# Optimization experiments

Measured on AMD Instinct MI355X. Metric: run time of the kernel, lower is better.

## Reference

```python
import jax, jax.numpy as jnp
import numpy as np

B, S, D_MODEL = 4, 2048, 128
NUM_HEADS, HEAD_DIM = 4, 32
EPS = 1e-6


def setup_inputs() -> dict:
    key = jax.random.key(0)
    ks = jax.random.split(key, 5)
    scale = 1.0 / np.sqrt(D_MODEL)
    return {
        "x": jax.random.normal(ks[0], (B, S, D_MODEL), dtype=jnp.float32),
        "Wq": jax.random.normal(ks[1], (D_MODEL, NUM_HEADS * HEAD_DIM), dtype=jnp.float32) * scale,
        "bq": jnp.zeros((NUM_HEADS * HEAD_DIM,), dtype=jnp.float32),
        "Wk": jax.random.normal(ks[2], (D_MODEL, NUM_HEADS * HEAD_DIM), dtype=jnp.float32) * scale,
        "bk": jnp.zeros((NUM_HEADS * HEAD_DIM,), dtype=jnp.float32),
        "Wv": jax.random.normal(ks[3], (D_MODEL, NUM_HEADS * HEAD_DIM), dtype=jnp.float32) * scale,
        "bv": jnp.zeros((NUM_HEADS * HEAD_DIM,), dtype=jnp.float32),
        "gamma": jnp.ones((D_MODEL,), dtype=jnp.float32),
        "beta": jnp.zeros((D_MODEL,), dtype=jnp.float32),
        "Wo": jax.random.normal(ks[4], (NUM_HEADS * HEAD_DIM, D_MODEL), dtype=jnp.float32) * scale,
        "bo": jnp.zeros((D_MODEL,), dtype=jnp.float32),
    }


def _split_heads(t):
    # [B, S, H*D] -> [B, H, S, D]
    b, s, _ = t.shape
    return t.reshape(b, s, NUM_HEADS, HEAD_DIM).transpose(0, 2, 1, 3)


def reference(x, Wq, bq, Wk, bk, Wv, bv, gamma, beta, Wo, bo):
    # Pre-LayerNorm (Keras LayerNormalization, eps=1e-6)
    mu = jnp.mean(x, axis=-1, keepdims=True)
    var = jnp.mean(jnp.square(x - mu), axis=-1, keepdims=True)
    xn = (x - mu) * jax.lax.rsqrt(var + EPS) * gamma + beta

    q = _split_heads(xn @ Wq + bq)  # [B,H,S,Dh]
    k = _split_heads(xn @ Wk + bk)
    v = _split_heads(xn @ Wv + bv)

    scores = jnp.einsum("bhqd,bhkd->bhqk", q, k) / jnp.sqrt(jnp.float32(HEAD_DIM))
    attn = jax.nn.softmax(scores, axis=-1)  # [B,H,S,S]
    ctx = jnp.einsum("bhqk,bhkd->bhqd", attn, v)  # [B,H,S,Dh]

    # merge heads -> [B,S,H*Dh]
    ctx = ctx.transpose(0, 2, 1, 3).reshape(x.shape[0], x.shape[1], NUM_HEADS * HEAD_DIM)
    out = ctx @ Wo + bo
    return out + x  # residual
```

## Files before the change

### kernel.cpp

```cpp
#include <hip/hip_runtime.h>

#define D_MODEL 128
#define SEQ 2048
#define NH 4
#define DH 32
#define NBATCH 4
#define BHN 16

typedef __attribute__((ext_vector_type(8))) short bf16x8;
typedef __attribute__((ext_vector_type(4))) float f32x4;
typedef __attribute__((ext_vector_type(4))) unsigned short u16x4;
typedef __attribute__((ext_vector_type(8))) unsigned short u16x8;

#define QSCALE (0.17677669529663687f * 1.4426950408889634f)

static __device__ __forceinline__ unsigned short f2bf_rne(float f) {
    union { float f; unsigned int u; } v; v.f = f;
    unsigned int r = v.u + 0x7FFFu + ((v.u >> 16) & 1u);
    return (unsigned short)(r >> 16);
}


__global__ __launch_bounds__(512) void k1_ln_qkv(
    const float* __restrict__ x,
    const float* __restrict__ Wq, const float* __restrict__ Wk,
    const float* __restrict__ Wv,
    const float* __restrict__ bq, const float* __restrict__ bk,
    const float* __restrict__ bv,
    const float* __restrict__ gamma, const float* __restrict__ beta,
    unsigned short* __restrict__ qf_ws, unsigned short* __restrict__ kf_ws,
    unsigned short* __restrict__ vf_ws)
{
    __shared__ __align__(16) unsigned short wsh[96 * 512];
    __shared__ __align__(16) unsigned short xsh[32][136];
    __shared__ __align__(16) unsigned short stqk[32][272];
    __shared__ __align__(16) unsigned short stv[128][40];
    const int t = threadIdx.x, w = t >> 6, lane = t & 63;
    const int col = lane & 15, quad = lane >> 4;
    const int row0 = blockIdx.x * 32;
    const float g0 = gamma[lane], g1 = gamma[lane + 64];
    const float be0 = beta[lane], be1 = beta[lane + 64];
    #pragma unroll
    for (int i = 0; i < 4; ++i) {
        int r = w * 4 + i;
        const float* xr = x + (size_t)(row0 + r) * 128;
        float x0 = xr[lane], x1 = xr[lane + 64];
        float s = x0 + x1, s2 = x0 * x0 + x1 * x1;
        #pragma unroll
        for (int off = 32; off > 0; off >>= 1) {
            s += __shfl_xor(s, off);
            s2 += __shfl_xor(s2, off);
        }
        float mu  = s * (1.0f / 128.0f);
        float var = s2 * (1.0f / 128.0f) - mu * mu;
        float rs  = rsqrtf(var + 1e-6f);
        xsh[r][lane]      = f2bf_rne((x0 - mu) * rs * g0 + be0);
        xsh[r][lane + 64] = f2bf_rne((x1 - mu) * rs * g1 + be1);
    }

    #pragma unroll
    for (int i = 0; i < 12; ++i) {
        int u = w * 12 + i;
        int nt = u >> 2, kk = u & 3;
        const float* W = (nt < 8) ? Wq : (nt < 16) ? Wk : Wv;
        int n = (nt & 7) * 16 + col;
        u16x8 v;
        #pragma unroll
        for (int j = 0; j < 8; ++j)
            v[j] = f2bf_rne(W[(kk * 32 + quad * 8 + j) * 128 + n]);
        *(u16x8*)&wsh[(size_t)u * 512 + lane * 8] = v;
    }
    __syncthreads();

    const int mt = w & 1, mrow = mt * 16;
    const int nt0 = (w >> 1) * 6;
    bf16x8 a[4];
    #pragma unroll
    for (int kk = 0; kk < 4; ++kk)
        a[kk] = *(const bf16x8*)&xsh[mrow + col][kk * 32 + quad * 8];

    for (int nt = nt0; nt < nt0 + 6; ++nt) {
        int n = nt * 16 + col;
        f32x4 c = {0.f, 0.f, 0.f, 0.f};
        #pragma unroll
        for (int kk = 0; kk < 4; ++kk) {
            bf16x8 bfr = *(const bf16x8*)&wsh[(size_t)(nt * 4 + kk) * 512 + lane * 8];
            c = __builtin_amdgcn_mfma_f32_16x16x32_bf16(a[kk], bfr, c, 0, 0, 0);
        }
        int m = nt >> 3;
        int nn = n & 127;
        if (m < 2) {
            float bias = (m == 0) ? bq[nn] : bk[nn];
            float scale = (m == 0) ? QSCALE : 1.0f;
            #pragma unroll
            for (int r = 0; r < 4; ++r)
                stqk[mrow + quad * 4 + r][n] = f2bf_rne((c[r] + bias) * scale);
        } else {
            float bias = bv[nn];
            u16x4 pv;
            #pragma unroll
            for (int r = 0; r < 4; ++r) pv[r] = f2bf_rne(c[r] + bias);
            *(u16x4*)&stv[nn][mrow + quad * 4] = pv;
        }
    }
    __syncthreads();

    const int b   = row0 >> 11;
    const int kbi = (row0 & (SEQ - 1)) >> 5;
    const int h   = w >> 1, par = w & 1;
    const int bh  = b * NH + h;
    {
        u16x8 qv = *(const u16x8*)&stqk[par * 16 + col][h * 32 + quad * 8];
        int qi = ((row0 & (SEQ - 1)) >> 4) + par;
        *(u16x8*)(qf_ws + (size_t)(bh * 128 + qi) * 512 + lane * 8) = qv;
    }
    {
        u16x8 kv = *(const u16x8*)&stqk[2 * col + par][128 + h * 32 + quad * 8];
        *(u16x8*)(kf_ws + ((size_t)(bh * 64 + kbi) * 2 + par) * 512 + lane * 8) = kv;
    }
    {
        u16x8 vv = *(const u16x8*)&stv[h * 32 + par * 16 + col][quad * 8];
        *(u16x8*)(vf_ws + ((size_t)(bh * 64 + kbi) * 2 + par) * 512 + lane * 8) = vv;
    }
}

__global__ __launch_bounds__(1024) void k23_attn_out(
    const unsigned short* __restrict__ qf_ws,
    const unsigned short* __restrict__ kf_ws,
    const unsigned short* __restrict__ vf_ws,
    const float* __restrict__ Wo,
    const float* __restrict__ bo, const float* __restrict__ x,
    float* __restrict__ out)
{
    __shared__ __align__(16) unsigned short wo_sh[32 * 512];
    __shared__ __align__(16) float comb[16][32][33];
    __shared__ float lsh[16][32];
    __shared__ __align__(16) unsigned short ctx_sh[32][136];

    const int w = threadIdx.x >> 6, lane = threadIdx.x & 63;
    const int col = lane & 15, quad = lane >> 4;
    const int h = w >> 2, kh = w & 3;
    const int b = blockIdx.y;
    const int bh = b * NH + h;
    const int q0 = blockIdx.x * 32;
    const int qi = blockIdx.x * 2;

    #pragma unroll
    for (int i = 0; i < 2; ++i) {
        int u = w * 2 + i;
        int nt = u >> 2, kk = u & 3;
        int n = nt * 16 + col;
        u16x8 vv;
        #pragma unroll
        for (int j = 0; j < 8; ++j)
            vv[j] = f2bf_rne(Wo[(kk * 32 + quad * 8 + j) * 128 + n]);
        *(u16x8*)&wo_sh[(size_t)u * 512 + lane * 8] = vv;
    }

    const unsigned short* qb = qf_ws + (size_t)(bh * 128 + qi) * 512;
    const unsigned short* kb0 = kf_ws + (size_t)bh * 65536 + (size_t)(kh * 16) * 1024;
    const unsigned short* vb0 = vf_ws + (size_t)bh * 65536 + (size_t)(kh * 16) * 1024;

    bf16x8 qf0 = *(const bf16x8*)(qb + lane * 8);
    bf16x8 qf1 = *(const bf16x8*)(qb + 512 + lane * 8);

    f32x4 c00 = {0.f,0.f,0.f,0.f}, c01 = {0.f,0.f,0.f,0.f};
    f32x4 c10 = {0.f,0.f,0.f,0.f}, c11 = {0.f,0.f,0.f,0.f};
    float l0 = 0.f, l1 = 0.f;

    const unsigned short* pk = kb0;
    const unsigned short* pv = vb0;
    bf16x8 kf0 = *(const bf16x8*)(pk + lane * 8);
    bf16x8 kf1 = *(const bf16x8*)(pk + 512 + lane * 8);
    bf16x8 vf0 = *(const bf16x8*)(pv + lane * 8);
    bf16x8 vf1 = *(const bf16x8*)(pv + 512 + lane * 8);

    for (int it = 0; it < 16; ++it) {
        const unsigned short* nk = (it == 15) ? kb0 : pk + 1024;
        const unsigned short* nv = (it == 15) ? vb0 : pv + 1024;
        bf16x8 nkf0 = *(const bf16x8*)(nk + lane * 8);
        bf16x8 nkf1 = *(const bf16x8*)(nk + 512 + lane * 8);
        bf16x8 nvf0 = *(const bf16x8*)(nv + lane * 8);
        bf16x8 nvf1 = *(const bf16x8*)(nv + 512 + lane * 8);

        f32x4 z = {0.f,0.f,0.f,0.f};
        __builtin_amdgcn_s_setprio(1);
        f32x4 s00 = __builtin_amdgcn_mfma_f32_16x16x32_bf16(kf0, qf0, z, 0, 0, 0);
        f32x4 s01 = __builtin_amdgcn_mfma_f32_16x16x32_bf16(kf1, qf0, z, 0, 0, 0);
        f32x4 s10 = __builtin_amdgcn_mfma_f32_16x16x32_bf16(kf0, qf1, z, 0, 0, 0);
        f32x4 s11 = __builtin_amdgcn_mfma_f32_16x16x32_bf16(kf1, qf1, z, 0, 0, 0);
        __builtin_amdgcn_s_setprio(0);

        union { bf16x8 v; unsigned int u[4]; } pf0, pf1;
        #pragma unroll
        for (int r = 0; r < 4; ++r) {
            float pe = __builtin_amdgcn_exp2f(s00[r]);
            float po = __builtin_amdgcn_exp2f(s01[r]);
            l0 += pe + po;
            pf0.u[r] = (__float_as_uint(pe) >> 16) | (__float_as_uint(po) & 0xFFFF0000u);
            float qe = __builtin_amdgcn_exp2f(s10[r]);
            float qo = __builtin_amdgcn_exp2f(s11[r]);
            l1 += qe + qo;
            pf1.u[r] = (__float_as_uint(qe) >> 16) | (__float_as_uint(qo) & 0xFFFF0000u);
        }
        __builtin_amdgcn_s_setprio(1);
        c00 = __builtin_amdgcn_mfma_f32_16x16x32_bf16(pf0.v, vf0, c00, 0, 0, 0);
        c01 = __builtin_amdgcn_mfma_f32_16x16x32_bf16(pf0.v, vf1, c01, 0, 0, 0);
        c10 = __builtin_amdgcn_mfma_f32_16x16x32_bf16(pf1.v, vf0, c10, 0, 0, 0);
        c11 = __builtin_amdgcn_mfma_f32_16x16x32_bf16(pf1.v, vf1, c11, 0, 0, 0);
        __builtin_amdgcn_s_setprio(0);
        kf0 = nkf0; kf1 = nkf1; vf0 = nvf0; vf1 = nvf1;
        pk = nk; pv = nv;
    }

    l0 += __shfl_xor(l0, 16); l0 += __shfl_xor(l0, 32);
    l1 += __shfl_xor(l1, 16); l1 += __shfl_xor(l1, 32);

    #pragma unroll
    for (int r = 0; r < 4; ++r) {
        int rr = quad * 4 + r;
        comb[w][rr][col]           = c00[r];
        comb[w][rr][16 + col]      = c01[r];
        comb[w][16 + rr][col]      = c10[r];
        comb[w][16 + rr][16 + col] = c11[r];
    }
    if (quad == 0) {
        lsh[w][col]      = l0;
        lsh[w][16 + col] = l1;
    }
    __syncthreads();

    {
        int row = threadIdx.x >> 5;
        int dg  = (threadIdx.x & 31) * 4;
        int hh  = dg >> 5;
        int wb  = hh * 4;
        float linv = 1.0f / (lsh[wb][row] + lsh[wb + 1][row]
                           + lsh[wb + 2][row] + lsh[wb + 3][row]);
        int dl = dg & 31;
        u16x4 ov;
        #pragma unroll
        for (int j = 0; j < 4; ++j)
            ov[j] = f2bf_rne((comb[wb][row][dl + j] + comb[wb + 1][row][dl + j]
                            + comb[wb + 2][row][dl + j] + comb[wb + 3][row][dl + j])
                             * linv);
        *(u16x4*)&ctx_sh[row][dg] = ov;
    }
    __syncthreads();

    {
        int nt = w & 7, mt = w >> 3;
        bf16x8 a[4];
        #pragma unroll
        for (int kk = 0; kk < 4; ++kk)
            a[kk] = *(const bf16x8*)&ctx_sh[mt * 16 + col][kk * 32 + quad * 8];
        int n = nt * 16 + col;
        f32x4 c = {0.f, 0.f, 0.f, 0.f};
        #pragma unroll
        for (int kk = 0; kk < 4; ++kk) {
            bf16x8 bfr = *(const bf16x8*)&wo_sh[(size_t)(nt * 4 + kk) * 512 + lane * 8];
            c = __builtin_amdgcn_mfma_f32_16x16x32_bf16(a[kk], bfr, c, 0, 0, 0);
        }
        float bias = bo[n];
        #pragma unroll
        for (int r = 0; r < 4; ++r) {
            size_t row_g = (size_t)b * SEQ + q0 + mt * 16 + quad * 4 + r;
            out[row_g * 128 + n] = c[r] + bias + x[row_g * 128 + n];
        }
    }
}

extern "C" void kernel_launch(void* const* d_in, const int* in_sizes, int n_in,
                              void* d_out, int out_size, void* d_ws, size_t ws_size,
                              hipStream_t stream) {
    const float* x     = (const float*)d_in[0];
    const float* Wq    = (const float*)d_in[1];
    const float* bq    = (const float*)d_in[2];
    const float* Wk    = (const float*)d_in[3];
    const float* bk    = (const float*)d_in[4];
    const float* Wv    = (const float*)d_in[5];
    const float* bv    = (const float*)d_in[6];
    const float* gamma = (const float*)d_in[7];
    const float* beta  = (const float*)d_in[8];
    const float* Wo    = (const float*)d_in[9];
    const float* bo    = (const float*)d_in[10];
    float* out = (float*)d_out;

    const size_t QKV_ELEMS = (size_t)BHN * SEQ * DH;
    unsigned short* qf_ws = (unsigned short*)d_ws;
    unsigned short* kf_ws = qf_ws + QKV_ELEMS;
    unsigned short* vf_ws = kf_ws + QKV_ELEMS;

    k1_ln_qkv<<<256, 512, 0, stream>>>(x, Wq, Wk, Wv, bq, bk, bv, gamma, beta,
                                       qf_ws, kf_ws, vf_ws);
    k23_attn_out<<<dim3(64, 4), 1024, 0, stream>>>(qf_ws, kf_ws, vf_ws, Wo,
                                                   bo, x, out);
}
```

Baseline: 100.2 us.

## Swizzle blocks across XCDs per batch and use packed bf16 conversion

Both kernels move to a 1D grid. Block IDs are remapped so that all blocks working on one batch land on the same pair of XCDs, which is meant to keep that batch's K/V and x rows resident in the shared L2. The LayerNorm stage now loads x, gamma and beta as float2 and writes packed bf16 pairs. The softmax probability packing swaps manual truncation for the hardware round-to-nearest pack2 conversion, which slightly changes rounding and may lower ALU cost in the inner loop.

```diff
diff --git a/kernel.cpp b/kernel.cpp
--- a/kernel.cpp
+++ b/kernel.cpp
@@ -1,4 +1,5 @@
 #include <hip/hip_runtime.h>
+#include <hip/hip_bf16.h>
 
 #define D_MODEL 128
 #define SEQ 2048
@@ -18,6 +19,13 @@
     union { float f; unsigned int u; } v; v.f = f;
     unsigned int r = v.u + 0x7FFFu + ((v.u >> 16) & 1u);
     return (unsigned short)(r >> 16);
+}
+
+static __device__ __forceinline__ unsigned int pack2_bf16(float lo, float hi) {
+    float2 t; t.x = lo; t.y = hi;
+    union { __hip_bfloat162 b; unsigned int u; } cv;
+    cv.b = __float22bfloat162_rn(t);
+    return cv.u;
 }
 
 
@@ -37,14 +45,21 @@
     __shared__ __align__(16) unsigned short stv[128][40];
     const int t = threadIdx.x, w = t >> 6, lane = t & 63;
     const int col = lane & 15, quad = lane >> 4;
-    const int row0 = blockIdx.x * 32;
-    const float g0 = gamma[lane], g1 = gamma[lane + 64];
-    const float be0 = beta[lane], be1 = beta[lane + 64];
+
+    const int bid = blockIdx.x;
+    const int xcd = bid & 7, slot = bid >> 3;
+    const int bsw = xcd >> 1;
+    const int rblk = (xcd & 1) * 32 + slot;
+    const int row0 = bsw * SEQ + rblk * 32;
+
+    const float2 gg = ((const float2*)gamma)[lane];
+    const float2 bb = ((const float2*)beta)[lane];
     #pragma unroll
     for (int i = 0; i < 4; ++i) {
         int r = w * 4 + i;
         const float* xr = x + (size_t)(row0 + r) * 128;
-        float x0 = xr[lane], x1 = xr[lane + 64];
+        float2 xp = ((const float2*)xr)[lane];
+        float x0 = xp.x, x1 = xp.y;
         float s = x0 + x1, s2 = x0 * x0 + x1 * x1;
         #pragma unroll
         for (int off = 32; off > 0; off >>= 1) {
@@ -54,8 +69,9 @@
         float mu  = s * (1.0f / 128.0f);
         float var = s2 * (1.0f / 128.0f) - mu * mu;
         float rs  = rsqrtf(var + 1e-6f);
-        xsh[r][lane]      = f2bf_rne((x0 - mu) * rs * g0 + be0);
-        xsh[r][lane + 64] = f2bf_rne((x1 - mu) * rs * g1 + be1);
+        *(unsigned int*)&xsh[r][lane * 2] =
+            pack2_bf16((x0 - mu) * rs * gg.x + bb.x,
+                       (x1 - mu) * rs * gg.y + bb.y);
     }
 
     #pragma unroll
@@ -140,10 +156,14 @@
     const int w = threadIdx.x >> 6, lane = threadIdx.x & 63;
     const int col = lane & 15, quad = lane >> 4;
     const int h = w >> 2, kh = w & 3;
-    const int b = blockIdx.y;
+
+    const int bid = blockIdx.x;
+    const int xcd = bid & 7, slot = bid >> 3;
+    const int b = xcd >> 1;
+    const int qib = (xcd & 1) * 32 + slot;
     const int bh = b * NH + h;
-    const int q0 = blockIdx.x * 32;
-    const int qi = blockIdx.x * 2;
+    const int q0 = qib * 32;
+    const int qi = qib * 2;
 
     #pragma unroll
     for (int i = 0; i < 2; ++i) {
@@ -197,11 +217,11 @@
             float pe = __builtin_amdgcn_exp2f(s00[r]);
             float po = __builtin_amdgcn_exp2f(s01[r]);
             l0 += pe + po;
-            pf0.u[r] = (__float_as_uint(pe) >> 16) | (__float_as_uint(po) & 0xFFFF0000u);
+            pf0.u[r] = pack2_bf16(pe, po);
             float qe = __builtin_amdgcn_exp2f(s10[r]);
             float qo = __builtin_amdgcn_exp2f(s11[r]);
             l1 += qe + qo;
-            pf1.u[r] = (__float_as_uint(qe) >> 16) | (__float_as_uint(qo) & 0xFFFF0000u);
+            pf1.u[r] = pack2_bf16(qe, qo);
         }
         __builtin_amdgcn_s_setprio(1);
         c00 = __builtin_amdgcn_mfma_f32_16x16x32_bf16(pf0.v, vf0, c00, 0, 0, 0);
@@ -293,6 +313,6 @@
 
     k1_ln_qkv<<<256, 512, 0, stream>>>(x, Wq, Wk, Wv, bq, bk, bv, gamma, beta,
                                        qf_ws, kf_ws, vf_ws);
-    k23_attn_out<<<dim3(64, 4), 1024, 0, stream>>>(qf_ws, kf_ws, vf_ws, Wo,
-                                                   bo, x, out);
-}
+    k23_attn_out<<<256, 1024, 0, stream>>>(qf_ws, kf_ws, vf_ws, Wo,
+                                           bo, x, out);
+}
```

New measurement: 103.2 us. +2.9%, slower.

## Fuse LN-QKV and attention kernels into one cooperative kernel with grid sync

Applied to the files above, without the earlier changes.

Merges the LayerNorm+QKV projection kernel and the attention+output-projection kernel into a single cooperative launch of 256 blocks of 1024 threads, separated by a grid-wide barrier. Shared memory is aliased between the two phases, and the Wo staging is done before the barrier to overlap with the QKV writes. This removes one kernel launch and the gap between kernels. In exchange it adds a grid sync and requires all 256 blocks to be co-resident, and the first phase now runs with doubled block size.

```diff
diff --git a/kernel.cpp b/kernel.cpp
--- a/kernel.cpp
+++ b/kernel.cpp
@@ -1,4 +1,7 @@
 #include <hip/hip_runtime.h>
+#include <hip/hip_cooperative_groups.h>
+
+namespace cg = cooperative_groups;
 
 #define D_MODEL 128
 #define SEQ 2048
@@ -21,46 +24,58 @@
 }
 
 
-__global__ __launch_bounds__(512) void k1_ln_qkv(
+__global__ __launch_bounds__(1024) void fused_mha(
     const float* __restrict__ x,
     const float* __restrict__ Wq, const float* __restrict__ Wk,
-    const float* __restrict__ Wv,
+    const float* __restrict__ Wv, const float* __restrict__ Wo,
     const float* __restrict__ bq, const float* __restrict__ bk,
-    const float* __restrict__ bv,
+    const float* __restrict__ bv, const float* __restrict__ bo,
     const float* __restrict__ gamma, const float* __restrict__ beta,
     unsigned short* __restrict__ qf_ws, unsigned short* __restrict__ kf_ws,
-    unsigned short* __restrict__ vf_ws)
+    unsigned short* __restrict__ vf_ws, float* __restrict__ out)
 {
-    __shared__ __align__(16) unsigned short wsh[96 * 512];
-    __shared__ __align__(16) unsigned short xsh[32][136];
-    __shared__ __align__(16) unsigned short stqk[32][272];
-    __shared__ __align__(16) unsigned short stv[128][40];
+    __shared__ __align__(16) char smemA[98304];
+    __shared__ __align__(16) char smemB[36864];
+
+    unsigned short* wsh = (unsigned short*)smemA;
+    auto xsh  = (unsigned short (*)[136])(smemB);
+    auto stqk = (unsigned short (*)[272])(smemB + 8704);
+    auto stv  = (unsigned short (*)[40]) (smemB + 26112);
+    unsigned short* wo_sh = (unsigned short*)smemB;
+    auto comb = (float (*)[32][33])(smemA);
+    auto lsh  = (float (*)[32])(smemA + 67584);
+    auto ctx_sh = (unsigned short (*)[136])(smemA + 69632);
+
     const int t = threadIdx.x, w = t >> 6, lane = t & 63;
     const int col = lane & 15, quad = lane >> 4;
-    const int row0 = blockIdx.x * 32;
-    const float g0 = gamma[lane], g1 = gamma[lane + 64];
-    const float be0 = beta[lane], be1 = beta[lane + 64];
+    const int bid = blockIdx.x;
+    const int row0 = bid * 32;
+
+    {
+        const float g0 = gamma[lane], g1 = gamma[lane + 64];
+        const float be0 = beta[lane], be1 = beta[lane + 64];
+        #pragma unroll
+        for (int i = 0; i < 2; ++i) {
+            int r = w * 2 + i;
+            const float* xr = x + (size_t)(row0 + r) * 128;
+            float x0 = xr[lane], x1 = xr[lane + 64];
+            float s = x0 + x1, s2 = x0 * x0 + x1 * x1;
+            #pragma unroll
+            for (int off = 32; off > 0; off >>= 1) {
+                s += __shfl_xor(s, off);
+                s2 += __shfl_xor(s2, off);
+            }
+            float mu  = s * (1.0f / 128.0f);
+            float var = s2 * (1.0f / 128.0f) - mu * mu;
+            float rs  = rsqrtf(var + 1e-6f);
+            xsh[r][lane]      = f2bf_rne((x0 - mu) * rs * g0 + be0);
+            xsh[r][lane + 64] = f2bf_rne((x1 - mu) * rs * g1 + be1);
+        }
+    }
+
     #pragma unroll
-    for (int i = 0; i < 4; ++i) {
-        int r = w * 4 + i;
-        const float* xr = x + (size_t)(row0 + r) * 128;
-        float x0 = xr[lane], x1 = xr[lane + 64];
-        float s = x0 + x1, s2 = x0 * x0 + x1 * x1;
-        #pragma unroll
-        for (int off = 32; off > 0; off >>= 1) {
-            s += __shfl_xor(s, off);
-            s2 += __shfl_xor(s2, off);
-        }
-        float mu  = s * (1.0f / 128.0f);
-        float var = s2 * (1.0f / 128.0f) - mu * mu;
-        float rs  = rsqrtf(var + 1e-6f);
-        xsh[r][lane]      = f2bf_rne((x0 - mu) * rs * g0 + be0);
-        xsh[r][lane + 64] = f2bf_rne((x1 - mu) * rs * g1 + be1);
-    }
-
-    #pragma unroll
-    for (int i = 0; i < 12; ++i) {
-        int u = w * 12 + i;
+    for (int i = 0; i < 6; ++i) {
+        int u = w * 6 + i;
         int nt = u >> 2, kk = u & 3;
         const float* W = (nt < 8) ? Wq : (nt < 16) ? Wk : Wv;
         int n = (nt & 7) * 16 + col;
@@ -72,78 +87,63 @@
     }
     __syncthreads();
 
-    const int mt = w & 1, mrow = mt * 16;
-    const int nt0 = (w >> 1) * 6;
-    bf16x8 a[4];
-    #pragma unroll
-    for (int kk = 0; kk < 4; ++kk)
-        a[kk] = *(const bf16x8*)&xsh[mrow + col][kk * 32 + quad * 8];
-
-    for (int nt = nt0; nt < nt0 + 6; ++nt) {
-        int n = nt * 16 + col;
-        f32x4 c = {0.f, 0.f, 0.f, 0.f};
-        #pragma unroll
-        for (int kk = 0; kk < 4; ++kk) {
-            bf16x8 bfr = *(const bf16x8*)&wsh[(size_t)(nt * 4 + kk) * 512 + lane * 8];
-            c = __builtin_amdgcn_mfma_f32_16x16x32_bf16(a[kk], bfr, c, 0, 0, 0);
-        }
-        int m = nt >> 3;
-        int nn = n & 127;
-        if (m < 2) {
-            float bias = (m == 0) ? bq[nn] : bk[nn];
-            float scale = (m == 0) ? QSCALE : 1.0f;
+    {
+        const int mt = w & 1, mrow = mt * 16;
+        const int nt0 = (w >> 1) * 3;
+        bf16x8 a[4];
+        #pragma unroll
+        for (int kk = 0; kk < 4; ++kk)
+            a[kk] = *(const bf16x8*)&xsh[mrow + col][kk * 32 + quad * 8];
+
+        for (int nt = nt0; nt < nt0 + 3; ++nt) {
+            int n = nt * 16 + col;
+            f32x4 c = {0.f, 0.f, 0.f, 0.f};
             #pragma unroll
-            for (int r = 0; r < 4; ++r)
-                stqk[mrow + quad * 4 + r][n] = f2bf_rne((c[r] + bias) * scale);
+            for (int kk = 0; kk < 4; ++kk) {
+                bf16x8 bfr = *(const bf16x8*)&wsh[(size_t)(nt * 4 + kk) * 512 + lane * 8];
+                c = __builtin_amdgcn_mfma_f32_16x16x32_bf16(a[kk], bfr, c, 0, 0, 0);
+            }
+            int m = nt >> 3;
+            int nn = n & 127;
+            if (m < 2) {
+                float bias = (m == 0) ? bq[nn] : bk[nn];
+                float scale = (m == 0) ? QSCALE : 1.0f;
+                #pragma unroll
+                for (int r = 0; r < 4; ++r)
+                    stqk[mrow + quad * 4 + r][n] = f2bf_rne((c[r] + bias) * scale);
+            } else {
+                float bias = bv[nn];
+                u16x4 pv;
+                #pragma unroll
+                for (int r = 0; r < 4; ++r) pv[r] = f2bf_rne(c[r] + bias);
+                *(u16x4*)&stv[nn][mrow + quad * 4] = pv;
+            }
+        }
+    }
+    __syncthreads();
+
+    {
+        const int b   = row0 >> 11;
+        const int kbi = (row0 & (SEQ - 1)) >> 5;
+        const int ws8 = w & 7;
+        const int h   = ws8 >> 1, par = ws8 & 1;
+        const int bh  = b * NH + h;
+        if (w < 8) {
+            {
+                u16x8 qv = *(const u16x8*)&stqk[par * 16 + col][h * 32 + quad * 8];
+                int qi = ((row0 & (SEQ - 1)) >> 4) + par;
+                *(u16x8*)(qf_ws + (size_t)(bh * 128 + qi) * 512 + lane * 8) = qv;
+            }
+            {
+                u16x8 kv = *(const u16x8*)&stqk[2 * col + par][128 + h * 32 + quad * 8];
+                *(u16x8*)(kf_ws + ((size_t)(bh * 64 + kbi) * 2 + par) * 512 + lane * 8) = kv;
+            }
         } else {
-            float bias = bv[nn];
-            u16x4 pv;
-            #pragma unroll
-            for (int r = 0; r < 4; ++r) pv[r] = f2bf_rne(c[r] + bias);
-            *(u16x4*)&stv[nn][mrow + quad * 4] = pv;
-        }
-    }
-    __syncthreads();
-
-    const int b   = row0 >> 11;
-    const int kbi = (row0 & (SEQ - 1)) >> 5;
-    const int h   = w >> 1, par = w & 1;
-    const int bh  = b * NH + h;
-    {
-        u16x8 qv = *(const u16x8*)&stqk[par * 16 + col][h * 32 + quad * 8];
-        int qi = ((row0 & (SEQ - 1)) >> 4) + par;
-        *(u16x8*)(qf_ws + (size_t)(bh * 128 + qi) * 512 + lane * 8) = qv;
-    }
-    {
-        u16x8 kv = *(const u16x8*)&stqk[2 * col + par][128 + h * 32 + quad * 8];
-        *(u16x8*)(kf_ws + ((size_t)(bh * 64 + kbi) * 2 + par) * 512 + lane * 8) = kv;
-    }
-    {
-        u16x8 vv = *(const u16x8*)&stv[h * 32 + par * 16 + col][quad * 8];
-        *(u16x8*)(vf_ws + ((size_t)(bh * 64 + kbi) * 2 + par) * 512 + lane * 8) = vv;
-    }
-}
-
-__global__ __launch_bounds__(1024) void k23_attn_out(
-    const unsigned short* __restrict__ qf_ws,
-    const unsigned short* __restrict__ kf_ws,
-    const unsigned short* __restrict__ vf_ws,
-    const float* __restrict__ Wo,
-    const float* __restrict__ bo, const float* __restrict__ x,
-    float* __restrict__ out)
-{
-    __shared__ __align__(16) unsigned short wo_sh[32 * 512];
-    __shared__ __align__(16) float comb[16][32][33];
-    __shared__ float lsh[16][32];
-    __shared__ __align__(16) unsigned short ctx_sh[32][136];
-
-    const int w = threadIdx.x >> 6, lane = threadIdx.x & 63;
-    const int col = lane & 15, quad = lane >> 4;
-    const int h = w >> 2, kh = w & 3;
-    const int b = blockIdx.y;
-    const int bh = b * NH + h;
-    const int q0 = blockIdx.x * 32;
-    const int qi = blockIdx.x * 2;
+            u16x8 vv = *(const u16x8*)&stv[h * 32 + par * 16 + col][quad * 8];
+            *(u16x8*)(vf_ws + ((size_t)(bh * 64 + kbi) * 2 + par) * 512 + lane * 8) = vv;
+        }
+    }
+    __syncthreads();
 
     #pragma unroll
     for (int i = 0; i < 2; ++i) {
@@ -156,6 +156,16 @@
             vv[j] = f2bf_rne(Wo[(kk * 32 + quad * 8 + j) * 128 + n]);
         *(u16x8*)&wo_sh[(size_t)u * 512 + lane * 8] = vv;
     }
+
+    __threadfence();
+    cg::this_grid().sync();
+
+    const int h = w >> 2, kh = w & 3;
+    const int b = bid >> 6;
+    const int qib = bid & 63;
+    const int bh = b * NH + h;
+    const int q0 = qib * 32;
+    const int qi = qib * 2;
 
     const unsigned short* qb = qf_ws + (size_t)(bh * 128 + qi) * 512;
     const unsigned short* kb0 = kf_ws + (size_t)bh * 65536 + (size_t)(kh * 16) * 1024;
@@ -291,8 +301,12 @@
     unsigned short* kf_ws = qf_ws + QKV_ELEMS;
     unsigned short* vf_ws = kf_ws + QKV_ELEMS;
 
-    k1_ln_qkv<<<256, 512, 0, stream>>>(x, Wq, Wk, Wv, bq, bk, bv, gamma, beta,
-                                       qf_ws, kf_ws, vf_ws);
-    k23_attn_out<<<dim3(64, 4), 1024, 0, stream>>>(qf_ws, kf_ws, vf_ws, Wo,
-                                                   bo, x, out);
+    void* args[] = {
+        (void*)&x, (void*)&Wq, (void*)&Wk, (void*)&Wv, (void*)&Wo,
+        (void*)&bq, (void*)&bk, (void*)&bv, (void*)&bo,
+        (void*)&gamma, (void*)&beta,
+        (void*)&qf_ws, (void*)&kf_ws, (void*)&vf_ws, (void*)&out
+    };
+    hipLaunchCooperativeKernel((const void*)fused_mha, dim3(256), dim3(1024),
+                               args, 0, stream);
 }
```

Measured after the change: 198.0 us. +97.6%, slower.
